# Kernel tuning notes

Hardware: AMD Instinct MI355X
Metric: run time of the kernel (lower is better)

Reference implementation:

```python
import jax, jax.numpy as jnp
import numpy as np

EPS = 1e-12  # F.normalize eps

def _l2norm(v):
    n = jnp.sqrt(jnp.sum(v * v, axis=-1, keepdims=True))
    return v / jnp.maximum(n, EPS)

def setup_inputs() -> dict:
    key = jax.random.key(0)
    k1, k2, k3 = jax.random.split(key, 3)
    B, C, H, Wd = 32, 256, 64, 64
    M = 64
    x = jax.random.normal(k1, (B, C, H, Wd), dtype=jnp.float32)
    stdv = 1.0 / np.sqrt(M)
    W = jax.random.uniform(k2, (M, C), dtype=jnp.float32, minval=-stdv, maxval=stdv)
    label_batch = jax.random.randint(k3, (B,), 0, 2)
    return {"x": x, "W": W, "label_batch": label_batch}

def reference(x, W, label_batch):
    B, C, H, Wd = x.shape
    M = W.shape[0]
    # [B, HW, C] tokens; key == query == flattened input (pos=False)
    tok = x.transpose(0, 2, 3, 1).reshape(B, H * Wd, C)
    # per-pixel contribution to each prototype, softmax over pixels (dim=1)
    proto_weight = jax.nn.softmax(jnp.einsum('bnc,mc->bnm', tok, W), axis=1)
    # prototypes [B, M, C], L2-normalized
    proto = _l2norm(jnp.einsum('bnm,bnc->bmc', proto_weight, tok))
    # relevance of each pixel to each prototype, softmax over prototypes
    score = jax.nn.softmax(jnp.einsum('bnc,bmc->bnm', tok, proto), axis=-1)
    # reconstructed query
    new_query = _l2norm(jnp.einsum('bnm,bmc->bnc', score, proto))
    # compact loss: MSE(keys, nearest prototype) (new_cpt == 'True')
    top1 = jnp.argmax(score, axis=-1)                      # [B, HW]
    pos = jnp.take_along_axis(proto, top1[:, :, None], axis=1)  # [B, HW, C]
    compact_loss = jnp.mean((tok - pos) ** 2)
    # distance loss: push prototypes apart
    p2 = jnp.sum(proto * proto, axis=-1)                   # [B, M]
    sqd = p2[:, :, None] + p2[:, None, :] - 2.0 * jnp.einsum('bmc,bkc->bmk', proto, proto)
    dis = 1.0 - sqd
    dis = dis * (dis > 0).astype(dis.dtype)
    dis = jnp.triu(dis, k=1)
    dis_loss = jnp.mean(jnp.sum(dis, axis=(1, 2)) * 2.0 / (M * (M - 1)))
    out = new_query.transpose(0, 2, 1).reshape(B, C, H, Wd)
    return (out, compact_loss, dis_loss)
```

## Files before the change

### kernel.cpp

```cpp
#include <hip/hip_runtime.h>
#include <math.h>

#define B 32
#define C 256
#define M 64
#define N 4096

typedef __attribute__((ext_vector_type(8))) short s16x8;
typedef __attribute__((ext_vector_type(8))) __bf16 bf16x8;
typedef __attribute__((ext_vector_type(4))) float f32x4;
typedef __attribute__((ext_vector_type(4))) unsigned short u16x4;
typedef __attribute__((ext_vector_type(8))) unsigned short u16x8;

static constexpr float EPS = 1e-12f;

__device__ __forceinline__ unsigned short f2bf(float f) {
    unsigned u = __float_as_uint(f);
    u += 0x7FFFu + ((u >> 16) & 1u);
    return (unsigned short)(u >> 16);
}
__device__ __forceinline__ float bf2f(unsigned short h) {
    return __uint_as_float((unsigned)h << 16);
}
__device__ __forceinline__ f32x4 MFMA(s16x8 a, s16x8 b, f32x4 c) {
    return __builtin_amdgcn_mfma_f32_16x16x32_bf16(
        __builtin_bit_cast(bf16x8, a), __builtin_bit_cast(bf16x8, b), c, 0, 0, 0);
}
__device__ __forceinline__ s16x8 cvt8(const f32x4 a, const f32x4 b) {
    bf16x8 h;
    h[0] = (__bf16)a[0]; h[1] = (__bf16)a[1]; h[2] = (__bf16)a[2]; h[3] = (__bf16)a[3];
    h[4] = (__bf16)b[0]; h[5] = (__bf16)b[1]; h[6] = (__bf16)b[2]; h[7] = (__bf16)b[3];
    return __builtin_bit_cast(s16x8, h);
}
__device__ __forceinline__ int swz(int n) {
    return (((n >> 2) & 3) | ((n & 1) << 2)) << 3;
}

__global__ __launch_bounds__(256) void kW_convert(const float* __restrict__ Wf,
                                                  unsigned short* __restrict__ Wb) {
    const int i = blockIdx.x * 256 + threadIdx.x;
    Wb[i] = f2bf(Wf[i]);
}

__global__ __launch_bounds__(256) void k01(const float* __restrict__ x,
                                           const unsigned short* __restrict__ Wb,
                                           unsigned short* __restrict__ xbt,
                                           unsigned short* __restrict__ Sb,
                                           float* __restrict__ xsq) {
    const int nb = blockIdx.x, b = blockIdx.y;
    const int t = threadIdx.x;
    __shared__ unsigned short tsT[64 * 256];
    __shared__ float xred[16][68];
    const int g = t & 15, cp = t >> 4;
    float part[4] = {0.f, 0.f, 0.f, 0.f};
    const float* xrow = x + (size_t)b * C * N + (size_t)nb * 64 + 4 * g;
#pragma unroll
    for (int i = 0; i < 16; ++i) {
        const int c = cp + 16 * i;
        const f32x4 q = *(const f32x4*)(xrow + (size_t)c * N);
#pragma unroll
        for (int k = 0; k < 4; ++k) {
            const float v = q[k];
            part[k] += v * v;
            const int n = 4 * g + k;
            tsT[n * 256 + (c ^ swz(n))] = f2bf(v);
        }
    }
#pragma unroll
    for (int k = 0; k < 4; ++k) xred[cp][4 * g + k] = part[k];
    __syncthreads();
    if (t < 64) {
        float s = 0.f;
#pragma unroll
        for (int j = 0; j < 16; ++j) s += xred[j][t];
        xsq[(size_t)b * N + nb * 64 + t] = s;
    }
    {
        const int l = t & 31, nh = t >> 5;
#pragma unroll
        for (int j = 0; j < 8; ++j) {
            const int n = nh + 8 * j;
            const int c0 = l * 8;
            const u16x8 v = *(const u16x8*)(&tsT[n * 256 + (c0 ^ swz(n))]);
            *(u16x8*)(xbt + ((size_t)b * N + nb * 64 + n) * C + c0) = v;
        }
    }
    const int wv = t >> 6, lane = t & 63, li = lane & 15, lk = lane >> 4;
    const f32x4 zv = {0.f, 0.f, 0.f, 0.f};
    f32x4 acc[4] = {zv, zv, zv, zv};
    const unsigned short* br = Wb + (size_t)(wv * 16 + li) * C + lk * 8;
#pragma unroll
    for (int c0 = 0; c0 < C; c0 += 32) {
        const s16x8 bfrag = *(const s16x8*)(br + c0);
#pragma unroll
        for (int s = 0; s < 4; ++s) {
            const int n = s * 16 + li;
            const s16x8 a = *(const s16x8*)(&tsT[n * 256 + ((lk * 8 + c0) ^ swz(n))]);
            acc[s] = MFMA(a, bfrag, acc[s]);
        }
    }
    unsigned short* Srow = Sb + ((size_t)b * M + wv * 16 + li) * N + nb * 64;
#pragma unroll
    for (int s = 0; s < 4; ++s) {
        u16x4 h;
#pragma unroll
        for (int r = 0; r < 4; ++r) h[r] = f2bf(acc[s][r]);
        *(u16x4*)(Srow + s * 16 + lk * 4) = h;
    }
}

__global__ __launch_bounds__(256) void k2_softmax_n(const unsigned short* __restrict__ Sb,
                                                    unsigned short* __restrict__ Pb) {
    const int m = blockIdx.x, b = blockIdx.y;
    const unsigned short* col = Sb + ((size_t)b * M + m) * N;
    unsigned short* po = Pb + ((size_t)b * M + m) * N;
    const int t = threadIdx.x;
    float v[16];
    const u16x8 h0 = *(const u16x8*)(col + t * 16);
    const u16x8 h1 = *(const u16x8*)(col + t * 16 + 8);
#pragma unroll
    for (int i = 0; i < 8; ++i) v[i] = bf2f(h0[i]);
#pragma unroll
    for (int i = 0; i < 8; ++i) v[8 + i] = bf2f(h1[i]);
    float mx = -INFINITY;
#pragma unroll
    for (int i = 0; i < 16; ++i) mx = fmaxf(mx, v[i]);
#pragma unroll
    for (int off = 32; off >= 1; off >>= 1) mx = fmaxf(mx, __shfl_xor(mx, off));
    __shared__ float redm[4], reds[4];
    const int wave = t >> 6, lane = t & 63;
    if (lane == 0) redm[wave] = mx;
    __syncthreads();
    mx = fmaxf(fmaxf(redm[0], redm[1]), fmaxf(redm[2], redm[3]));
    float s = 0.f;
#pragma unroll
    for (int i = 0; i < 16; ++i) {
        v[i] = __expf(v[i] - mx);
        s += v[i];
    }
#pragma unroll
    for (int off = 32; off >= 1; off >>= 1) s += __shfl_xor(s, off);
    if (lane == 0) reds[wave] = s;
    __syncthreads();
    s = reds[0] + reds[1] + reds[2] + reds[3];
    const float inv = 1.f / s;
    u16x8 o0, o1;
#pragma unroll
    for (int i = 0; i < 8; ++i) o0[i] = f2bf(v[i] * inv);
#pragma unroll
    for (int i = 0; i < 8; ++i) o1[i] = f2bf(v[8 + i] * inv);
    *(u16x8*)(po + t * 16) = o0;
    *(u16x8*)(po + t * 16 + 8) = o1;
}

__global__ __launch_bounds__(256) void k3_mfma(const float* __restrict__ x,
                                               const unsigned short* __restrict__ Pb,
                                               float* __restrict__ parts) {
    const int ck = blockIdx.x, b = blockIdx.y;
    const int wv = threadIdx.x >> 6, lane = threadIdx.x & 63;
    const int li = lane & 15, lk = lane >> 4;
    const int c0w = wv * 64;
    const int nb = ck * 512;
    const f32x4 zv = {0.f, 0.f, 0.f, 0.f};
    f32x4 acc[4][4];
#pragma unroll
    for (int s = 0; s < 4; ++s)
#pragma unroll
        for (int u = 0; u < 4; ++u) acc[s][u] = zv;
    const float* ar = x + ((size_t)b * C + c0w + li) * N + nb + lk * 8;
    const unsigned short* br = Pb + ((size_t)b * M + li) * N + nb + lk * 8;
#pragma unroll 4
    for (int n0 = 0; n0 < 512; n0 += 32) {
        s16x8 af[4], bf_[4];
#pragma unroll
        for (int s = 0; s < 4; ++s) {
            const float* p = ar + (size_t)(s * 16) * N + n0;
            af[s] = cvt8(*(const f32x4*)p, *(const f32x4*)(p + 4));
        }
#pragma unroll
        for (int u = 0; u < 4; ++u) bf_[u] = *(const s16x8*)(br + (size_t)(u * 16) * N + n0);
#pragma unroll
        for (int s = 0; s < 4; ++s)
#pragma unroll
            for (int u = 0; u < 4; ++u) acc[s][u] = MFMA(af[s], bf_[u], acc[s][u]);
    }
    float* pp = parts + ((size_t)b * 8 + ck) * M * C;
#pragma unroll
    for (int s = 0; s < 4; ++s)
#pragma unroll
        for (int u = 0; u < 4; ++u)
            *(f32x4*)(pp + (size_t)(u * 16 + li) * C + c0w + s * 16 + lk * 4) = acc[s][u];
}

__global__ __launch_bounds__(256) void k3b_reduce(const float* __restrict__ parts,
                                                  unsigned short* __restrict__ proto_bf,
                                                  unsigned short* __restrict__ protoT_bf,
                                                  float* __restrict__ p2) {
    const int mb = blockIdx.x, b = blockIdx.y;
    const int t = threadIdx.x;
    const int ml = t >> 5, cl = t & 31;
    const int m = mb * 8 + ml;
    const int c0 = cl * 8;
    float v[8] = {0.f, 0.f, 0.f, 0.f, 0.f, 0.f, 0.f, 0.f};
    const float* pbase = parts + (size_t)b * 8 * M * C + (size_t)m * C + c0;
#pragma unroll
    for (int ck = 0; ck < 8; ++ck) {
        const f32x4 q0 = *(const f32x4*)(pbase + (size_t)ck * M * C);
        const f32x4 q1 = *(const f32x4*)(pbase + (size_t)ck * M * C + 4);
#pragma unroll
        for (int j = 0; j < 4; ++j) { v[j] += q0[j]; v[4 + j] += q1[j]; }
    }
    float sq = 0.f;
#pragma unroll
    for (int j = 0; j < 8; ++j) sq += v[j] * v[j];
#pragma unroll
    for (int off = 16; off >= 1; off >>= 1) sq += __shfl_xor(sq, off);
    const float denom = fmaxf(sqrtf(sq), EPS);
    const float scale = 1.f / denom;
    if (cl == 0) p2[b * M + m] = sq / (denom * denom);
    u16x8 h;
#pragma unroll
    for (int j = 0; j < 8; ++j) h[j] = f2bf(v[j] * scale);
    *(u16x8*)(proto_bf + ((size_t)b * M + m) * C + c0) = h;
#pragma unroll
    for (int j = 0; j < 8; ++j)
        protoT_bf[((size_t)b * C + c0 + j) * M + m] = h[j];
}

__global__ __launch_bounds__(256) void k4_score(const unsigned short* __restrict__ proto_bf,
                                                const unsigned short* __restrict__ xbt,
                                                const float* __restrict__ p2,
                                                const float* __restrict__ xsq,
                                                unsigned short* __restrict__ pnm,
                                                float* __restrict__ cparts) {
    const int b = blockIdx.y;
    const int wv = threadIdx.x >> 6, lane = threadIdx.x & 63;
    const int li = lane & 15, lk = lane >> 4;
    const int nbase = blockIdx.x * 256 + wv * 64;
    const f32x4 zv = {0.f, 0.f, 0.f, 0.f};
    f32x4 acc[4][4];
#pragma unroll
    for (int s = 0; s < 4; ++s)
#pragma unroll
        for (int u = 0; u < 4; ++u) acc[s][u] = zv;
    const unsigned short* ar = proto_bf + ((size_t)b * M + li) * C + lk * 8;
    const unsigned short* br = xbt + ((size_t)b * N + nbase + li) * C + lk * 8;
#pragma unroll
    for (int c0 = 0; c0 < C; c0 += 32) {
        s16x8 af[4], bf_[4];
#pragma unroll
        for (int s = 0; s < 4; ++s) af[s] = *(const s16x8*)(ar + (size_t)(s * 16) * C + c0);
#pragma unroll
        for (int u = 0; u < 4; ++u) bf_[u] = *(const s16x8*)(br + (size_t)(u * 16) * C + c0);
#pragma unroll
        for (int s = 0; s < 4; ++s)
#pragma unroll
            for (int u = 0; u < 4; ++u) acc[s][u] = MFMA(af[s], bf_[u], acc[s][u]);
    }
    float csum = 0.f;
#pragma unroll
    for (int u = 0; u < 4; ++u) {
        const int n = nbase + u * 16 + li;
        float vmax = -INFINITY;
#pragma unroll
        for (int s = 0; s < 4; ++s)
#pragma unroll
            for (int r = 0; r < 4; ++r) vmax = fmaxf(vmax, acc[s][u][r]);
        vmax = fmaxf(vmax, __shfl_xor(vmax, 16));
        vmax = fmaxf(vmax, __shfl_xor(vmax, 32));
        int t1 = 1 << 30;
#pragma unroll
        for (int s = 0; s < 4; ++s)
#pragma unroll
            for (int r = 0; r < 4; ++r)
                if (acc[s][u][r] == vmax) t1 = min(t1, s * 16 + lk * 4 + r);
        t1 = min(t1, __shfl_xor(t1, 16));
        t1 = min(t1, __shfl_xor(t1, 32));
        float es = 0.f;
#pragma unroll
        for (int s = 0; s < 4; ++s)
#pragma unroll
            for (int r = 0; r < 4; ++r) {
                const float e = __expf(acc[s][u][r] - vmax);
                acc[s][u][r] = e;
                es += e;
            }
        es += __shfl_xor(es, 16);
        es += __shfl_xor(es, 32);
        const float inv = 1.f / es;
        unsigned short* prow = pnm + ((size_t)b * N + n) * M;
#pragma unroll
        for (int s = 0; s < 4; ++s) {
            u16x4 h;
#pragma unroll
            for (int r = 0; r < 4; ++r) h[r] = f2bf(acc[s][u][r] * inv);
            *(u16x4*)(prow + s * 16 + lk * 4) = h;
        }
        if (lk == 0) csum += xsq[(size_t)b * N + n] - 2.f * vmax + p2[b * M + t1];
    }
#pragma unroll
    for (int off = 32; off >= 1; off >>= 1) csum += __shfl_xor(csum, off);
    __shared__ float red[4];
    if (lane == 0) red[wv] = csum;
    __syncthreads();
    if (threadIdx.x == 0)
        cparts[b * 16 + blockIdx.x] = red[0] + red[1] + red[2] + red[3];
}

__global__ __launch_bounds__(256) void k4b_mfma(const unsigned short* __restrict__ pnm,
                                                const unsigned short* __restrict__ protoT_bf,
                                                float* __restrict__ out) {
    const int b = blockIdx.y;
    const int wv = threadIdx.x >> 6, lane = threadIdx.x & 63;
    const int li = lane & 15, lk = lane >> 4;
    const int n0 = blockIdx.x * 64;
    const int cb = wv * 64;
    const f32x4 zv = {0.f, 0.f, 0.f, 0.f};
    f32x4 acc[4][4];
#pragma unroll
    for (int s = 0; s < 4; ++s)
#pragma unroll
        for (int u = 0; u < 4; ++u) acc[s][u] = zv;
    const unsigned short* ar = pnm + ((size_t)b * N + n0 + li) * M + lk * 8;
    const unsigned short* br = protoT_bf + ((size_t)b * C + cb + li) * M + lk * 8;
#pragma unroll
    for (int m0 = 0; m0 < M; m0 += 32) {
        s16x8 af[4], bf_[4];
#pragma unroll
        for (int s = 0; s < 4; ++s) af[s] = *(const s16x8*)(ar + (size_t)(s * 16) * M + m0);
#pragma unroll
        for (int u = 0; u < 4; ++u) bf_[u] = *(const s16x8*)(br + (size_t)(u * 16) * M + m0);
#pragma unroll
        for (int s = 0; s < 4; ++s)
#pragma unroll
            for (int u = 0; u < 4; ++u) acc[s][u] = MFMA(af[s], bf_[u], acc[s][u]);
    }
    __shared__ float ls[4][64];
    __shared__ float ls2[64];
    float psq[4][4];
#pragma unroll
    for (int s = 0; s < 4; ++s)
#pragma unroll
        for (int r = 0; r < 4; ++r) {
            float sum = 0.f;
#pragma unroll
            for (int u = 0; u < 4; ++u) sum += acc[s][u][r] * acc[s][u][r];
#pragma unroll
            for (int off = 8; off >= 1; off >>= 1) sum += __shfl_xor(sum, off);
            psq[s][r] = sum;
        }
    if (li == 0) {
#pragma unroll
        for (int s = 0; s < 4; ++s)
#pragma unroll
            for (int r = 0; r < 4; ++r) ls[wv][s * 16 + lk * 4 + r] = psq[s][r];
    }
    __syncthreads();
    if (threadIdx.x < 64) {
        const int tt = threadIdx.x;
        const float tot = ls[0][tt] + ls[1][tt] + ls[2][tt] + ls[3][tt];
        ls2[tt] = 1.f / fmaxf(sqrtf(tot), EPS);
    }
    __syncthreads();
    float scl[4][4];
#pragma unroll
    for (int s = 0; s < 4; ++s)
#pragma unroll
        for (int r = 0; r < 4; ++r) scl[s][r] = ls2[s * 16 + lk * 4 + r];
    float* ob = out + (size_t)b * C * N;
#pragma unroll
    for (int s = 0; s < 4; ++s)
#pragma unroll
        for (int u = 0; u < 4; ++u) {
            f32x4 q;
#pragma unroll
            for (int r = 0; r < 4; ++r) q[r] = acc[s][u][r] * scl[s][r];
            *(f32x4*)(ob + (size_t)(cb + u * 16 + li) * N + n0 + s * 16 + lk * 4) = q;
        }
}

__global__ __launch_bounds__(256) void k5_dis(const unsigned short* __restrict__ proto_bf,
                                              const float* __restrict__ p2,
                                              float* __restrict__ dparts) {
    const int q = blockIdx.x;
    const int b = blockIdx.y;
    const unsigned short* pr = proto_bf + (size_t)b * M * C;
    __shared__ float pl[M * C];
    for (int idx = threadIdx.x; idx < M * C; idx += 256) {
        int m = idx >> 8, c = idx & 255;
        pl[m * 256 + (c ^ (m & 31))] = bf2f(pr[idx]);
    }
    __syncthreads();
    float sum = 0.f;
    for (int k = 0; k < 2; ++k) {
        const int pair = q * 512 + k * 256 + threadIdx.x;
        const int i = pair >> 6, j = pair & 63;
        if (j > i) {
            float g = 0.f;
#pragma unroll 8
            for (int c = 0; c < C; ++c)
                g += pl[i * 256 + (c ^ (i & 31))] * pl[j * 256 + (c ^ (j & 31))];
            const float d = 1.f - (p2[b * M + i] + p2[b * M + j] - 2.f * g);
            sum += fmaxf(d, 0.f);
        }
    }
#pragma unroll
    for (int off = 32; off >= 1; off >>= 1) sum += __shfl_xor(sum, off);
    __shared__ float red[4];
    const int wave = threadIdx.x >> 6, lane = threadIdx.x & 63;
    if (lane == 0) red[wave] = sum;
    __syncthreads();
    if (threadIdx.x == 0) dparts[b * 8 + q] = red[0] + red[1] + red[2] + red[3];
}

__global__ __launch_bounds__(256) void k6_final(const float* __restrict__ cparts,
                                                const float* __restrict__ dparts,
                                                float* __restrict__ losses) {
    const int t = threadIdx.x;
    float cs = cparts[t] + cparts[t + 256];
    float ds = dparts[t];
#pragma unroll
    for (int off = 32; off >= 1; off >>= 1) {
        cs += __shfl_xor(cs, off);
        ds += __shfl_xor(ds, off);
    }
    __shared__ float rc[4], rd[4];
    const int wave = t >> 6, lane = t & 63;
    if (lane == 0) { rc[wave] = cs; rd[wave] = ds; }
    __syncthreads();
    if (t == 0) {
        const float ctot = rc[0] + rc[1] + rc[2] + rc[3];
        const float dtot = rd[0] + rd[1] + rd[2] + rd[3];
        losses[0] = ctot / ((float)B * (float)N * (float)C);
        losses[1] = dtot * (2.f / (float)(M * (M - 1))) / (float)B;
    }
}

extern "C" void kernel_launch(void* const* d_in, const int* in_sizes, int n_in,
                              void* d_out, int out_size, void* d_ws, size_t ws_size,
                              hipStream_t stream) {
    const float* x = (const float*)d_in[0];
    const float* Wf = (const float*)d_in[1];
    float* out = (float*)d_out;

    unsigned short* xbt = (unsigned short*)d_out;
    float* losses = out + (size_t)B * C * N;

    float* wsf = (float*)d_ws;
    unsigned short* Sbf = (unsigned short*)wsf;
    float* parts = wsf;
    unsigned short* Pbf = (unsigned short*)(wsf + 4194304);
    unsigned short* pnm = Pbf;
    float* xsq = wsf + 8388608;
    unsigned short* proto_bf = (unsigned short*)(wsf + 8519680);
    unsigned short* protoT_bf = (unsigned short*)(wsf + 8781824);
    unsigned short* Wb = (unsigned short*)(wsf + 9043968);
    float* p2 = wsf + 9052160;
    float* cparts = wsf + 9054208;
    float* dparts = wsf + 9054720;

    kW_convert<<<dim3(64), 256, 0, stream>>>(Wf, Wb);
    k01<<<dim3(N / 64, B), 256, 0, stream>>>(x, Wb, xbt, Sbf, xsq);
    k2_softmax_n<<<dim3(M, B), 256, 0, stream>>>(Sbf, Pbf);
    k3_mfma<<<dim3(8, B), 256, 0, stream>>>(x, Pbf, parts);
    k3b_reduce<<<dim3(8, B), 256, 0, stream>>>(parts, proto_bf, protoT_bf, p2);
    k4_score<<<dim3(N / 256, B), 256, 0, stream>>>(proto_bf, xbt, p2, xsq, pnm, cparts);
    k4b_mfma<<<dim3(N / 64, B), 256, 0, stream>>>(pnm, protoT_bf, out);
    k5_dis<<<dim3(8, B), 256, 0, stream>>>(proto_bf, p2, dparts);
    k6_final<<<1, 256, 0, stream>>>(cparts, dparts, losses);
}
```

Before: 178.0 us.

## Fuse score softmax and reconstruction into one kernel, vectorize k01 LDS stores

Adds a fused k4f kernel that computes pixel-prototype scores, the softmax over prototypes, top-1 compact-loss terms, and then the score×proto matmul with L2 normalization. The score matrix stays in shared memory and is never round-tripped through global memory. The path is used only when the workspace is large enough to hold xbt separately, with scratch buffers moved into the output region. k01 also now writes four channels at a time as packed 64-bit LDS stores instead of scalar 16-bit stores. The cost is 512-thread blocks with heavier register and LDS use, which may lower occupancy.

```diff
diff --git a/kernel.cpp b/kernel.cpp
--- a/kernel.cpp
+++ b/kernel.cpp
@@ -51,23 +51,29 @@
     const int t = threadIdx.x;
     __shared__ unsigned short tsT[64 * 256];
     __shared__ float xred[16][68];
-    const int g = t & 15, cp = t >> 4;
+    const int nq = t & 15, cq = t >> 4;
     float part[4] = {0.f, 0.f, 0.f, 0.f};
-    const float* xrow = x + (size_t)b * C * N + (size_t)nb * 64 + 4 * g;
-#pragma unroll
-    for (int i = 0; i < 16; ++i) {
-        const int c = cp + 16 * i;
-        const f32x4 q = *(const f32x4*)(xrow + (size_t)c * N);
+    const float* xrow = x + (size_t)b * C * N + (size_t)nb * 64 + 4 * nq;
+#pragma unroll
+    for (int step = 0; step < 4; ++step) {
+        const int c0 = cq * 4 + step * 64;
+        f32x4 q[4];
+#pragma unroll
+        for (int i = 0; i < 4; ++i) q[i] = *(const f32x4*)(xrow + (size_t)(c0 + i) * N);
 #pragma unroll
         for (int k = 0; k < 4; ++k) {
-            const float v = q[k];
-            part[k] += v * v;
-            const int n = 4 * g + k;
-            tsT[n * 256 + (c ^ swz(n))] = f2bf(v);
-        }
-    }
-#pragma unroll
-    for (int k = 0; k < 4; ++k) xred[cp][4 * g + k] = part[k];
+            const int n = 4 * nq + k;
+            u16x4 h;
+#pragma unroll
+            for (int i = 0; i < 4; ++i) {
+                part[k] += q[i][k] * q[i][k];
+                h[i] = f2bf(q[i][k]);
+            }
+            *(u16x4*)(&tsT[n * 256 + (c0 ^ swz(n))]) = h;
+        }
+    }
+#pragma unroll
+    for (int k = 0; k < 4; ++k) xred[cq][4 * nq + k] = part[k];
     __syncthreads();
     if (t < 64) {
         float s = 0.f;
@@ -225,6 +231,160 @@
 #pragma unroll
     for (int j = 0; j < 8; ++j)
         protoT_bf[((size_t)b * C + c0 + j) * M + m] = h[j];
+}
+
+__global__ __launch_bounds__(512) void k4f(const unsigned short* __restrict__ proto_bf,
+                                           const unsigned short* __restrict__ protoT_bf,
+                                           const unsigned short* __restrict__ xbt,
+                                           const float* __restrict__ p2,
+                                           const float* __restrict__ xsq,
+                                           float* __restrict__ out,
+                                           float* __restrict__ cparts) {
+    const int b = blockIdx.y;
+    const int t = threadIdx.x;
+    const int w = t >> 6, lane = t & 63, li = lane & 15, lk = lane >> 4;
+    const int nblk = blockIdx.x * 256;
+    __shared__ unsigned short p_lds[256 * 64];
+    __shared__ float red2[2][256];
+    __shared__ float red8[8];
+    const f32x4 zv = {0.f, 0.f, 0.f, 0.f};
+    f32x4 acc[4][2];
+#pragma unroll
+    for (int s = 0; s < 4; ++s)
+#pragma unroll
+        for (int u = 0; u < 2; ++u) acc[s][u] = zv;
+    const unsigned short* ar = proto_bf + (size_t)b * M * C + (size_t)li * C + lk * 8;
+    const unsigned short* br = xbt + ((size_t)b * N + nblk + w * 32 + li) * C + lk * 8;
+#pragma unroll
+    for (int c0 = 0; c0 < C; c0 += 32) {
+        s16x8 af[4], bf_[2];
+#pragma unroll
+        for (int s = 0; s < 4; ++s) af[s] = *(const s16x8*)(ar + (size_t)(s * 16) * C + c0);
+#pragma unroll
+        for (int u = 0; u < 2; ++u) bf_[u] = *(const s16x8*)(br + (size_t)(u * 16) * C + c0);
+#pragma unroll
+        for (int s = 0; s < 4; ++s)
+#pragma unroll
+            for (int u = 0; u < 2; ++u) acc[s][u] = MFMA(af[s], bf_[u], acc[s][u]);
+    }
+    float csum = 0.f;
+#pragma unroll
+    for (int u = 0; u < 2; ++u) {
+        const int n = nblk + w * 32 + u * 16 + li;
+        const int nl = w * 32 + u * 16 + li;
+        float vmax = -INFINITY;
+#pragma unroll
+        for (int s = 0; s < 4; ++s)
+#pragma unroll
+            for (int r = 0; r < 4; ++r) vmax = fmaxf(vmax, acc[s][u][r]);
+        vmax = fmaxf(vmax, __shfl_xor(vmax, 16));
+        vmax = fmaxf(vmax, __shfl_xor(vmax, 32));
+        int t1 = 1 << 30;
+#pragma unroll
+        for (int s = 0; s < 4; ++s)
+#pragma unroll
+            for (int r = 0; r < 4; ++r)
+                if (acc[s][u][r] == vmax) t1 = min(t1, s * 16 + lk * 4 + r);
+        t1 = min(t1, __shfl_xor(t1, 16));
+        t1 = min(t1, __shfl_xor(t1, 32));
+        float es = 0.f;
+#pragma unroll
+        for (int s = 0; s < 4; ++s)
+#pragma unroll
+            for (int r = 0; r < 4; ++r) {
+                const float e = __expf(acc[s][u][r] - vmax);
+                acc[s][u][r] = e;
+                es += e;
+            }
+        es += __shfl_xor(es, 16);
+        es += __shfl_xor(es, 32);
+        const float inv = 1.f / es;
+#pragma unroll
+        for (int s = 0; s < 4; ++s) {
+            u16x4 h;
+#pragma unroll
+            for (int r = 0; r < 4; ++r) h[r] = f2bf(acc[s][u][r] * inv);
+            const unsigned off =
+                (unsigned)((nl * 128 + ((s * 16 + lk * 4) << 1)) ^ ((nl & 7) << 4));
+            *(u16x4*)((char*)p_lds + off) = h;
+        }
+        if (lk == 0) csum += xsq[(size_t)b * N + n] - 2.f * vmax + p2[b * M + t1];
+    }
+#pragma unroll
+    for (int off = 32; off >= 1; off >>= 1) csum += __shfl_xor(csum, off);
+    if (lane == 0) red8[w] = csum;
+    __syncthreads();
+    if (t == 0) {
+        float cs = 0.f;
+#pragma unroll
+        for (int j = 0; j < 8; ++j) cs += red8[j];
+        cparts[b * 16 + blockIdx.x] = cs;
+    }
+    const int nq = w & 3, ch = w >> 2;
+    f32x4 a2[4][8];
+#pragma unroll
+    for (int s = 0; s < 4; ++s)
+#pragma unroll
+        for (int u = 0; u < 8; ++u) a2[s][u] = zv;
+    const unsigned short* br2 =
+        protoT_bf + ((size_t)b * C + ch * 128 + li) * M + lk * 8;
+#pragma unroll
+    for (int m0 = 0; m0 < M; m0 += 32) {
+        s16x8 af2[4], bf2[8];
+#pragma unroll
+        for (int s = 0; s < 4; ++s) {
+            const int nl = nq * 64 + s * 16 + li;
+            const unsigned off =
+                (unsigned)((nl * 128 + ((m0 + lk * 8) << 1)) ^ ((nl & 7) << 4));
+            af2[s] = *(const s16x8*)((const char*)p_lds + off);
+        }
+#pragma unroll
+        for (int u = 0; u < 8; ++u)
+            bf2[u] = *(const s16x8*)(br2 + (size_t)(u * 16) * M + m0);
+#pragma unroll
+        for (int s = 0; s < 4; ++s)
+#pragma unroll
+            for (int u = 0; u < 8; ++u) a2[s][u] = MFMA(af2[s], bf2[u], a2[s][u]);
+    }
+    float ssq[4][4];
+#pragma unroll
+    for (int s = 0; s < 4; ++s)
+#pragma unroll
+        for (int r = 0; r < 4; ++r) {
+            float sum = 0.f;
+#pragma unroll
+            for (int u = 0; u < 8; ++u) sum += a2[s][u][r] * a2[s][u][r];
+#pragma unroll
+            for (int off = 8; off >= 1; off >>= 1) sum += __shfl_xor(sum, off);
+            ssq[s][r] = sum;
+        }
+    if (li == 0) {
+#pragma unroll
+        for (int s = 0; s < 4; ++s)
+#pragma unroll
+            for (int r = 0; r < 4; ++r)
+                red2[ch][nq * 64 + s * 16 + lk * 4 + r] = ssq[s][r];
+    }
+    __syncthreads();
+    float scl[4][4];
+#pragma unroll
+    for (int s = 0; s < 4; ++s)
+#pragma unroll
+        for (int r = 0; r < 4; ++r) {
+            const int nl = nq * 64 + s * 16 + lk * 4 + r;
+            scl[s][r] = 1.f / fmaxf(sqrtf(red2[0][nl] + red2[1][nl]), EPS);
+        }
+    float* ob = out + (size_t)b * C * N;
+#pragma unroll
+    for (int s = 0; s < 4; ++s)
+#pragma unroll
+        for (int u = 0; u < 8; ++u) {
+            const int c = ch * 128 + u * 16 + li;
+            f32x4 q;
+#pragma unroll
+            for (int r = 0; r < 4; ++r) q[r] = a2[s][u][r] * scl[s][r];
+            *(f32x4*)(ob + (size_t)c * N + nblk + nq * 64 + s * 16 + lk * 4) = q;
+        }
 }
 
 __global__ __launch_bounds__(256) void k4_score(const unsigned short* __restrict__ proto_bf,
@@ -442,30 +602,55 @@
     const float* x = (const float*)d_in[0];
     const float* Wf = (const float*)d_in[1];
     float* out = (float*)d_out;
-
-    unsigned short* xbt = (unsigned short*)d_out;
+    float* wsf = (float*)d_ws;
     float* losses = out + (size_t)B * C * N;
 
-    float* wsf = (float*)d_ws;
-    unsigned short* Sbf = (unsigned short*)wsf;
-    float* parts = wsf;
-    unsigned short* Pbf = (unsigned short*)(wsf + 4194304);
-    unsigned short* pnm = Pbf;
-    float* xsq = wsf + 8388608;
-    unsigned short* proto_bf = (unsigned short*)(wsf + 8519680);
-    unsigned short* protoT_bf = (unsigned short*)(wsf + 8781824);
-    unsigned short* Wb = (unsigned short*)(wsf + 9043968);
-    float* p2 = wsf + 9052160;
-    float* cparts = wsf + 9054208;
-    float* dparts = wsf + 9054720;
-
-    kW_convert<<<dim3(64), 256, 0, stream>>>(Wf, Wb);
-    k01<<<dim3(N / 64, B), 256, 0, stream>>>(x, Wb, xbt, Sbf, xsq);
-    k2_softmax_n<<<dim3(M, B), 256, 0, stream>>>(Sbf, Pbf);
-    k3_mfma<<<dim3(8, B), 256, 0, stream>>>(x, Pbf, parts);
-    k3b_reduce<<<dim3(8, B), 256, 0, stream>>>(parts, proto_bf, protoT_bf, p2);
-    k4_score<<<dim3(N / 256, B), 256, 0, stream>>>(proto_bf, xbt, p2, xsq, pnm, cparts);
-    k4b_mfma<<<dim3(N / 64, B), 256, 0, stream>>>(pnm, protoT_bf, out);
-    k5_dis<<<dim3(8, B), 256, 0, stream>>>(proto_bf, p2, dparts);
-    k6_final<<<1, 256, 0, stream>>>(cparts, dparts, losses);
-}
+    const bool big = ws_size >= (size_t)69774336;
+
+    if (big) {
+        unsigned short* Sbf = (unsigned short*)out;
+        float* parts = out + 4194304;
+        unsigned short* Pbf = (unsigned short*)(out + 8388608);
+        unsigned short* xbt = (unsigned short*)wsf;
+        float* xsq = wsf + 16777216;
+        unsigned short* proto_bf = (unsigned short*)(wsf + 16908288);
+        unsigned short* protoT_bf = (unsigned short*)(wsf + 17170432);
+        unsigned short* Wb = (unsigned short*)(wsf + 17432576);
+        float* p2 = wsf + 17440768;
+        float* cparts = wsf + 17442816;
+        float* dparts = wsf + 17443328;
+
+        kW_convert<<<dim3(64), 256, 0, stream>>>(Wf, Wb);
+        k01<<<dim3(N / 64, B), 256, 0, stream>>>(x, Wb, xbt, Sbf, xsq);
+        k2_softmax_n<<<dim3(M, B), 256, 0, stream>>>(Sbf, Pbf);
+        k3_mfma<<<dim3(8, B), 256, 0, stream>>>(x, Pbf, parts);
+        k3b_reduce<<<dim3(8, B), 256, 0, stream>>>(parts, proto_bf, protoT_bf, p2);
+        k4f<<<dim3(N / 256, B), 512, 0, stream>>>(proto_bf, protoT_bf, xbt, p2, xsq,
+                                                  out, cparts);
+        k5_dis<<<dim3(8, B), 256, 0, stream>>>(proto_bf, p2, dparts);
+        k6_final<<<1, 256, 0, stream>>>(cparts, dparts, losses);
+    } else {
+        unsigned short* xbt = (unsigned short*)d_out;
+        unsigned short* Sbf = (unsigned short*)wsf;
+        float* parts = wsf;
+        unsigned short* Pbf = (unsigned short*)(wsf + 4194304);
+        unsigned short* pnm = Pbf;
+        float* xsq = wsf + 8388608;
+        unsigned short* proto_bf = (unsigned short*)(wsf + 8519680);
+        unsigned short* protoT_bf = (unsigned short*)(wsf + 8781824);
+        unsigned short* Wb = (unsigned short*)(wsf + 9043968);
+        float* p2 = wsf + 9052160;
+        float* cparts = wsf + 9054208;
+        float* dparts = wsf + 9054720;
+
+        kW_convert<<<dim3(64), 256, 0, stream>>>(Wf, Wb);
+        k01<<<dim3(N / 64, B), 256, 0, stream>>>(x, Wb, xbt, Sbf, xsq);
+        k2_softmax_n<<<dim3(M, B), 256, 0, stream>>>(Sbf, Pbf);
+        k3_mfma<<<dim3(8, B), 256, 0, stream>>>(x, Pbf, parts);
+        k3b_reduce<<<dim3(8, B), 256, 0, stream>>>(parts, proto_bf, protoT_bf, p2);
+        k4_score<<<dim3(N / 256, B), 256, 0, stream>>>(proto_bf, xbt, p2, xsq, pnm, cparts);
+        k4b_mfma<<<dim3(N / 64, B), 256, 0, stream>>>(pnm, protoT_bf, out);
+        k5_dis<<<dim3(8, B), 256, 0, stream>>>(proto_bf, p2, dparts);
+        k6_final<<<1, 256, 0, stream>>>(cparts, dparts, losses);
+    }
+}
```

New measurement: 194.7 us. 9.4% more time.
